# Kernel tuning notes

Hardware: AMD Instinct MI355X
Metric: run time of the kernel (lower is better)

## Reference

```python
import jax, jax.numpy as jnp
import numpy as np

B, R, C = 4, 36, 3          # batch, n_rotations, kernel_dim/output_dim
H, W = 384, 224             # padded image spatial: (320+64, 160+64)
CROP = 64
PAD = CROP // 2             # pad_size = 32


def setup_inputs() -> dict:
    key = jax.random.key(0)
    k1, k2 = jax.random.split(key)
    logits = jax.random.normal(k1, (B, C, H, W), dtype=jnp.float32)
    kernel = jax.random.normal(k2, (B * R, C, CROP, CROP), dtype=jnp.float32)
    return {"logits": logits, "kernel": kernel}


def _correlate(logits, kernel):
    # Original computes a full B x (B*R) cross-correlation via F.conv2d and then
    # discards all off-diagonal blocks. A grouped conv (feature_group_count=B)
    # computes exactly the kept diagonal blocks: group i correlates sample i's
    # feature map with that sample's R rotated kernels. interpolate/crop are
    # per-channel/per-pixel so they commute with the channel selection -> same math.
    b, c, h, w = logits.shape
    r = kernel.shape[0] // b
    x = logits.reshape(1, b * c, h, w)
    out = jax.lax.conv_general_dilated(
        x, kernel,
        window_strides=(1, 1),
        padding=[(PAD, PAD), (PAD, PAD)],
        dimension_numbers=("NCHW", "OIHW", "NCHW"),
        feature_group_count=b,
    )  # [1, b*r, h+1, w+1]  (h + 2*PAD - CROP + 1 = h + 1)
    out = out.reshape(b, r, out.shape[-2], out.shape[-1])
    # F.interpolate(..., mode='bilinear', align_corners=False) == half-pixel
    # bilinear resize without antialiasing.
    out = jax.image.resize(out, (b, r, h, w), method="bilinear", antialias=False)
    out = out[:, :, PAD:-PAD, PAD:-PAD]  # [b, r, h-2*PAD, w-2*PAD] = [b, r, 320, 160]
    hc, wc = out.shape[-2], out.shape[-1]
    # softmax over the flattened per-sample (rotation x spatial) map
    flat = jax.nn.softmax(out.reshape(b, -1), axis=-1)
    return flat.reshape(b, r, hc, wc)


def reference(logits, kernel):
    return _correlate(logits, kernel)
```

## Files before the change

### kernel.cpp

```cpp
#include <hip/hip_runtime.h>

typedef short bf16x8 __attribute__((ext_vector_type(8)));
typedef float f32x4  __attribute__((ext_vector_type(4)));
typedef unsigned short u16;

#define B_ 4
#define R_ 36
#define RP 48
#define C_ 3
#define H_ 384
#define W_ 224
#define KS 64
#define OY 321
#define OX 161
#define HC 320
#define WC 160
#define LCOLS 128
#define PITCH 88
#define CHUNK 6144
#define BLKS_PER_BATCH 7200

__device__ __forceinline__ u16 bf16rtn(float v) {
    union { float f; unsigned u; } U; U.f = v;
    unsigned r = U.u + 0x7fffu + ((U.u >> 16) & 1u);
    return (u16)(r >> 16);
}
__device__ __forceinline__ float bf16tof(u16 h) {
    union { float f; unsigned u; } U; U.u = ((unsigned)h) << 16; return U.f;
}

__device__ __forceinline__ float wave_max(float v) {
    #pragma unroll
    for (int off = 32; off > 0; off >>= 1) v = fmaxf(v, __shfl_down(v, off, 64));
    return v;
}
__device__ __forceinline__ float wave_sum(float v) {
    #pragma unroll
    for (int off = 32; off > 0; off >>= 1) v += __shfl_down(v, off, 64);
    return v;
}

__device__ __forceinline__ void dma16(const u16* g, u16* l) {
    __builtin_amdgcn_global_load_lds(
        (const __attribute__((address_space(1))) void*)g,
        (__attribute__((address_space(3))) void*)l, 16, 0, 0);
}

__global__ __launch_bounds__(256) void prep_weights(
    const float* __restrict__ wk, u16* __restrict__ wa)
{
    int d = blockIdx.x * 256 + threadIdx.x;
    int ky    = d & 63;
    int t1    = d >> 6;
    int r     = t1 % 48;
    int t2    = t1 / 48;
    int plane = t2 & 1;
    int t3    = t2 >> 1;
    int kx    = t3 & 63;
    int bc    = t3 >> 6;
    int c     = bc % 3;
    int b     = bc / 3;
    float v = 0.f;
    if (r < R_) v = wk[(((size_t)(b*R_ + r)*C_ + c)*KS + ky)*KS + kx];
    u16 h = bf16rtn(v);
    u16 o = plane ? bf16rtn(v - bf16tof(h)) : h;
    int kySw = ky ^ ((r & 7) << 3);
    wa[(size_t)t3*CHUNK + plane*3072 + r*64 + kySw] = o;
}

template<int NT>
__device__ __forceinline__ void conv_body(
    const float* __restrict__ in, const u16* __restrict__ wa,
    float* __restrict__ out, u16* Lh, u16* Ll, u16* Ab, int x0, int y0)
{
    const int b    = blockIdx.z;
    const int t    = threadIdx.x;
    const int w    = __builtin_amdgcn_readfirstlane(t >> 6);
    const int lane = t & 63;
    const int nu   = lane & 15;
    const int q    = lane >> 4;

    f32x4 acc[3][NT];
    #pragma unroll
    for (int mi = 0; mi < 3; mi++)
        #pragma unroll
        for (int n = 0; n < NT; n++)
            acc[mi][n] = (f32x4){0.f, 0.f, 0.f, 0.f};

    const u16* wbase = wa + (size_t)(b*192)*CHUNK;

    {
        const u16* src = wbase + (3*w)*512 + lane*8;
        u16* dst = Ab + (3*w)*512;
        dma16(src,        dst);
        dma16(src + 512,  dst + 512);
        dma16(src + 1024, dst + 1024);
    }

    for (int c = 0; c < C_; c++) {
        __syncthreads();
        const float* src = in + ((size_t)(b*C_ + c))*H_*W_;
        #pragma unroll
        for (int k = 0; k < 6; k++) {
            int idx = t + 256*k;
            if (idx < 1408) {
                int pair = idx >> 5;
                int r0   = pair * 2;
                int c4   = (idx & 31) * 4;
                int gx   = x0 + c4;
                int gy   = y0 + r0;
                float4 va = make_float4(0.f,0.f,0.f,0.f), vb = va;
                if (gx < W_) {
                    if (gy < H_)     va = *(const float4*)(src + (size_t)gy*W_ + gx);
                    if (gy + 1 < H_) vb = *(const float4*)(src + (size_t)(gy+1)*W_ + gx);
                }
                const float* pa = &va.x;
                const float* pb = &vb.x;
                #pragma unroll
                for (int j = 0; j < 4; j++) {
                    int col = c4 + j;
                    u16 ha = bf16rtn(pa[j]);
                    u16 hb = bf16rtn(pb[j]);
                    u16 la = bf16rtn(pa[j] - bf16tof(ha));
                    u16 lb = bf16rtn(pb[j] - bf16tof(hb));
                    *(unsigned*)&Lh[col*PITCH + r0] = (unsigned)ha | ((unsigned)hb << 16);
                    *(unsigned*)&Ll[col*PITCH + r0] = (unsigned)la | ((unsigned)lb << 16);
                }
            }
        }
        __syncthreads();

        #pragma unroll 1
        for (int kx = 0; kx < KS; kx++) {
            const int g = c*64 + kx;
            const int p = g & 1;
            __builtin_amdgcn_s_waitcnt(0x3F70);
            __builtin_amdgcn_s_barrier();
            if (g + 1 < 192) {
                const u16* s2 = wbase + (size_t)(g+1)*CHUNK + (3*w)*512 + lane*8;
                u16* d2 = Ab + (p^1)*CHUNK + (3*w)*512;
                dma16(s2,        d2);
                dma16(s2 + 512,  d2 + 512);
                dma16(s2 + 1024, d2 + 1024);
            }
            const u16* Abp = Ab + p*CHUNK;
            #pragma unroll
            for (int kycI = 0; kycI < 2; kycI++) {
                const int kyc = kycI * 32;
                bf16x8 Ah[3], Al[3];
                #pragma unroll
                for (int mi = 0; mi < 3; mi++) {
                    int off = (mi*16 + nu)*64 + ((kyc + 8*q) ^ ((nu & 7) << 3));
                    Ah[mi] = *(const bf16x8*)(Abp + off);
                    Al[mi] = *(const bf16x8*)(Abp + 3072 + off);
                }
                const u16* colbase = Lh + (size_t)(nu + kx)*PITCH + kyc + 8*q + 8*w;
                #pragma unroll
                for (int n = 0; n < NT; n++) {
                    const u16* ph = colbase + n*16*PITCH;
                    bf16x8 Bh = *(const bf16x8*)ph;
                    bf16x8 Bl = *(const bf16x8*)(ph + (size_t)LCOLS*PITCH);
                    #pragma unroll
                    for (int mi = 0; mi < 3; mi++) {
                        acc[mi][n] = __builtin_amdgcn_mfma_f32_16x16x32_bf16(Ah[mi], Bh, acc[mi][n], 0, 0, 0);
                        acc[mi][n] = __builtin_amdgcn_mfma_f32_16x16x32_bf16(Ah[mi], Bl, acc[mi][n], 0, 0, 0);
                        acc[mi][n] = __builtin_amdgcn_mfma_f32_16x16x32_bf16(Al[mi], Bh, acc[mi][n], 0, 0, 0);
                    }
                }
            }
        }
    }

    const int y = y0 + 8*w;
    if (y <= 320) {
        #pragma unroll
        for (int mi = 0; mi < 3; mi++) {
            #pragma unroll
            for (int n = 0; n < NT; n++) {
                #pragma unroll
                for (int i = 0; i < 4; i++) {
                    int r = mi*16 + q*4 + i;
                    int x = x0 + n*16 + nu;
                    if (r < R_ && x < OX)
                        out[((size_t)(b*R_ + r)*OY + y)*OX + x] = acc[mi][n][i];
                }
            }
        }
    }
}

__global__ __launch_bounds__(256) void conv_mfma(
    const float* __restrict__ in, const u16* __restrict__ wa, float* __restrict__ out)
{
    __shared__ __align__(16) u16 smem[2*LCOLS*PITCH + 2*CHUNK];
    u16* Lh = smem;
    u16* Ll = smem + LCOLS*PITCH;
    u16* Ab = smem + 2*LCOLS*PITCH;
    const int s  = blockIdx.y;
    const int y0 = (s < 80) ? (((s >> 3) << 5) + (s & 7)) : 320;

    if (blockIdx.x == 0)      conv_body<4>(in, wa, out, Lh, Ll, Ab, 0,   y0);
    else if (blockIdx.x == 1) conv_body<4>(in, wa, out, Lh, Ll, Ab, 64,  y0);
    else                      conv_body<3>(in, wa, out, Lh, Ll, Ab, 128, y0);
}

__global__ __launch_bounds__(256) void resize_kernel(
    const float* __restrict__ cv, float* __restrict__ out, float* __restrict__ pmax)
{
    const int t = threadIdx.x;
    const int idx = blockIdx.x * 256 + t;
    const int j = idx % WC;
    const int rest = idx / WC;
    const int i = rest % HC;
    const int br = rest / HC;

    float fy = (i + 32.5f) * (1.0f/384.0f);
    float fx = (j + 32.5f) * (1.0f/224.0f);

    const float* p = cv + ((size_t)br*OY + i)*OX + j;
    float v00 = p[0], v01 = p[1], v10 = p[OX], v11 = p[OX+1];
    float v = (1.f-fy)*((1.f-fx)*v00 + fx*v01) + fy*((1.f-fx)*v10 + fx*v11);
    out[idx] = v;

    __shared__ float sm[4];
    float m = wave_max(v);
    if ((t & 63) == 0) sm[t >> 6] = m;
    __syncthreads();
    if (t == 0) pmax[blockIdx.x] = fmaxf(fmaxf(sm[0], sm[1]), fmaxf(sm[2], sm[3]));
}

__global__ __launch_bounds__(256) void reduce_kernel(
    const float* __restrict__ part, float* __restrict__ res, int n, int is_sum)
{
    const int b = blockIdx.x;
    const int t = threadIdx.x;
    const float* p = part + (size_t)b*n;
    float v = is_sum ? 0.f : -3.0e38f;
    for (int k = t; k < n; k += 256) v = is_sum ? (v + p[k]) : fmaxf(v, p[k]);
    __shared__ float sm[4];
    float w = is_sum ? wave_sum(v) : wave_max(v);
    if ((t & 63) == 0) sm[t >> 6] = w;
    __syncthreads();
    if (t == 0) {
        res[b] = is_sum ? (sm[0]+sm[1]+sm[2]+sm[3])
                        : fmaxf(fmaxf(sm[0], sm[1]), fmaxf(sm[2], sm[3]));
    }
}

__global__ __launch_bounds__(256) void exp_kernel(
    float* __restrict__ out, const float* __restrict__ bmax, float* __restrict__ psum)
{
    const int t = threadIdx.x;
    const int idx = blockIdx.x * 256 + t;
    const int b = blockIdx.x / BLKS_PER_BATCH;
    float e = expf(out[idx] - bmax[b]);
    out[idx] = e;
    __shared__ float sm[4];
    float s = wave_sum(e);
    if ((t & 63) == 0) sm[t >> 6] = s;
    __syncthreads();
    if (t == 0) psum[blockIdx.x] = sm[0]+sm[1]+sm[2]+sm[3];
}

__global__ __launch_bounds__(256) void scale_kernel(
    float* __restrict__ out, const float* __restrict__ bsum)
{
    const int idx = blockIdx.x * 256 + threadIdx.x;
    const int b = blockIdx.x / BLKS_PER_BATCH;
    out[idx] = out[idx] / bsum[b];
}

extern "C" void kernel_launch(void* const* d_in, const int* in_sizes, int n_in,
                              void* d_out, int out_size, void* d_ws, size_t ws_size,
                              hipStream_t stream)
{
    const float* logits = (const float*)d_in[0];
    const float* wk     = (const float*)d_in[1];
    float* out = (float*)d_out;
    char*  wsB = (char*)d_ws;

    float* convOut = (float*)wsB;
    u16*   wa      = (u16*)(wsB + 29768256);
    float* pmax    = (float*)(wsB + 29768256 + 9437184);
    float* psum    = pmax + 28800;
    float* bmax    = psum + 28800;
    float* bsum    = bmax + 8;

    hipLaunchKernelGGL(prep_weights, dim3(18432), dim3(256), 0, stream, wk, wa);
    hipLaunchKernelGGL(conv_mfma,    dim3(3, 81, B_), dim3(256), 0, stream, logits, wa, convOut);
    hipLaunchKernelGGL(resize_kernel, dim3(28800), dim3(256), 0, stream, convOut, out, pmax);
    hipLaunchKernelGGL(reduce_kernel, dim3(4),     dim3(256), 0, stream, pmax, bmax, BLKS_PER_BATCH, 0);
    hipLaunchKernelGGL(exp_kernel,    dim3(28800), dim3(256), 0, stream, out, bmax, psum);
    hipLaunchKernelGGL(reduce_kernel, dim3(4),     dim3(256), 0, stream, psum, bsum, BLKS_PER_BATCH, 1);
    hipLaunchKernelGGL(scale_kernel,  dim3(28800), dim3(256), 0, stream, out, bsum);
}
```

Before: 703.1 us.

## Compute two output row groups per conv block to reuse weight tiles

```diff
diff --git a/kernel.cpp b/kernel.cpp
--- a/kernel.cpp
+++ b/kernel.cpp
@@ -16,8 +16,8 @@
 #define HC 320
 #define WC 160
 #define LCOLS 128
-#define PITCH 88
-#define CHUNK 6144
+#define PITCH 120
+#define GR 3072
 #define BLKS_PER_BATCH 7200
 
 __device__ __forceinline__ u16 bf16rtn(float v) {
@@ -50,22 +50,23 @@
     const float* __restrict__ wk, u16* __restrict__ wa)
 {
     int d = blockIdx.x * 256 + threadIdx.x;
-    int ky    = d & 63;
-    int t1    = d >> 6;
+    int ky32  = d & 31;
+    int t1    = d >> 5;
     int r     = t1 % 48;
     int t2    = t1 / 48;
     int plane = t2 & 1;
-    int t3    = t2 >> 1;
-    int kx    = t3 & 63;
-    int bc    = t3 >> 6;
+    int g2    = t2 >> 1;
+    int kycp  = g2 & 1;
+    int kx    = (g2 >> 1) & 63;
+    int bc    = g2 >> 7;
     int c     = bc % 3;
     int b     = bc / 3;
+    int ky    = kycp*32 + ky32;
     float v = 0.f;
     if (r < R_) v = wk[(((size_t)(b*R_ + r)*C_ + c)*KS + ky)*KS + kx];
     u16 h = bf16rtn(v);
     u16 o = plane ? bf16rtn(v - bf16tof(h)) : h;
-    int kySw = ky ^ ((r & 7) << 3);
-    wa[(size_t)t3*CHUNK + plane*3072 + r*64 + kySw] = o;
+    wa[(size_t)g2*GR + plane*1536 + r*32 + (ky32 ^ ((r & 3) << 3))] = o;
 }
 
 template<int NT>
@@ -80,30 +81,31 @@
     const int nu   = lane & 15;
     const int q    = lane >> 4;
 
-    f32x4 acc[3][NT];
+    f32x4 acc[2][3][NT];
     #pragma unroll
-    for (int mi = 0; mi < 3; mi++)
+    for (int yi = 0; yi < 2; yi++)
         #pragma unroll
-        for (int n = 0; n < NT; n++)
-            acc[mi][n] = (f32x4){0.f, 0.f, 0.f, 0.f};
-
-    const u16* wbase = wa + (size_t)(b*192)*CHUNK;
+        for (int mi = 0; mi < 3; mi++)
+            #pragma unroll
+            for (int n = 0; n < NT; n++)
+                acc[yi][mi][n] = (f32x4){0.f, 0.f, 0.f, 0.f};
+
+    const u16* gbase = wa + (size_t)(b*384)*GR;
 
     {
-        const u16* src = wbase + (3*w)*512 + lane*8;
-        u16* dst = Ab + (3*w)*512;
-        dma16(src,        dst);
-        dma16(src + 512,  dst + 512);
-        dma16(src + 1024, dst + 1024);
+        const u16* s0 = gbase + lane*8;
+        if (w < 2) { dma16(s0 + (2*w)*512, Ab + (2*w)*512);
+                     dma16(s0 + (2*w+1)*512, Ab + (2*w+1)*512); }
+        else       { dma16(s0 + (w+2)*512, Ab + (w+2)*512); }
     }
 
     for (int c = 0; c < C_; c++) {
         __syncthreads();
         const float* src = in + ((size_t)(b*C_ + c))*H_*W_;
         #pragma unroll
-        for (int k = 0; k < 6; k++) {
+        for (int k = 0; k < 8; k++) {
             int idx = t + 256*k;
-            if (idx < 1408) {
+            if (idx < 1920) {
                 int pair = idx >> 5;
                 int r0   = pair * 2;
                 int c4   = (idx & 31) * 4;
@@ -131,58 +133,62 @@
         __syncthreads();
 
         #pragma unroll 1
-        for (int kx = 0; kx < KS; kx++) {
-            const int g = c*64 + kx;
-            const int p = g & 1;
+        for (int gi = 0; gi < 128; gi++) {
+            const int g = c*128 + gi;
             __builtin_amdgcn_s_waitcnt(0x3F70);
             __builtin_amdgcn_s_barrier();
-            if (g + 1 < 192) {
-                const u16* s2 = wbase + (size_t)(g+1)*CHUNK + (3*w)*512 + lane*8;
-                u16* d2 = Ab + (p^1)*CHUNK + (3*w)*512;
-                dma16(s2,        d2);
-                dma16(s2 + 512,  d2 + 512);
-                dma16(s2 + 1024, d2 + 1024);
-            }
-            const u16* Abp = Ab + p*CHUNK;
+            if (g + 1 < 384) {
+                const u16* s2 = gbase + (size_t)(g+1)*GR + lane*8;
+                u16* d2 = Ab + ((g+1) & 1)*GR;
+                if (w < 2) { dma16(s2 + (2*w)*512, d2 + (2*w)*512);
+                             dma16(s2 + (2*w+1)*512, d2 + (2*w+1)*512); }
+                else       { dma16(s2 + (w+2)*512, d2 + (w+2)*512); }
+            }
+            const u16* Abp = Ab + (g & 1)*GR;
+            const int kx   = gi >> 1;
+            const int kycp = gi & 1;
+
+            bf16x8 Ah[3], Al[3];
             #pragma unroll
-            for (int kycI = 0; kycI < 2; kycI++) {
-                const int kyc = kycI * 32;
-                bf16x8 Ah[3], Al[3];
+            for (int mi = 0; mi < 3; mi++) {
+                int off = (mi*16 + nu)*32 + ((8*q) ^ ((nu & 3) << 3));
+                Ah[mi] = *(const bf16x8*)(Abp + off);
+                Al[mi] = *(const bf16x8*)(Abp + 1536 + off);
+            }
+            const u16* colbase = Lh + (size_t)(nu + kx)*PITCH + 32*kycp + 8*q + 8*w;
+            #pragma unroll
+            for (int n = 0; n < NT; n++) {
                 #pragma unroll
-                for (int mi = 0; mi < 3; mi++) {
-                    int off = (mi*16 + nu)*64 + ((kyc + 8*q) ^ ((nu & 7) << 3));
-                    Ah[mi] = *(const bf16x8*)(Abp + off);
-                    Al[mi] = *(const bf16x8*)(Abp + 3072 + off);
-                }
-                const u16* colbase = Lh + (size_t)(nu + kx)*PITCH + kyc + 8*q + 8*w;
-                #pragma unroll
-                for (int n = 0; n < NT; n++) {
-                    const u16* ph = colbase + n*16*PITCH;
+                for (int yi = 0; yi < 2; yi++) {
+                    const u16* ph = colbase + n*16*PITCH + 32*yi;
                     bf16x8 Bh = *(const bf16x8*)ph;
                     bf16x8 Bl = *(const bf16x8*)(ph + (size_t)LCOLS*PITCH);
                     #pragma unroll
                     for (int mi = 0; mi < 3; mi++) {
-                        acc[mi][n] = __builtin_amdgcn_mfma_f32_16x16x32_bf16(Ah[mi], Bh, acc[mi][n], 0, 0, 0);
-                        acc[mi][n] = __builtin_amdgcn_mfma_f32_16x16x32_bf16(Ah[mi], Bl, acc[mi][n], 0, 0, 0);
-                        acc[mi][n] = __builtin_amdgcn_mfma_f32_16x16x32_bf16(Al[mi], Bh, acc[mi][n], 0, 0, 0);
+                        acc[yi][mi][n] = __builtin_amdgcn_mfma_f32_16x16x32_bf16(Ah[mi], Bh, acc[yi][mi][n], 0, 0, 0);
+                        acc[yi][mi][n] = __builtin_amdgcn_mfma_f32_16x16x32_bf16(Ah[mi], Bl, acc[yi][mi][n], 0, 0, 0);
+                        acc[yi][mi][n] = __builtin_amdgcn_mfma_f32_16x16x32_bf16(Al[mi], Bh, acc[yi][mi][n], 0, 0, 0);
                     }
                 }
             }
         }
     }
 
-    const int y = y0 + 8*w;
-    if (y <= 320) {
-        #pragma unroll
-        for (int mi = 0; mi < 3; mi++) {
+    #pragma unroll
+    for (int yi = 0; yi < 2; yi++) {
+        const int y = y0 + 8*w + 32*yi;
+        if (y <= 320) {
             #pragma unroll
-            for (int n = 0; n < NT; n++) {
+            for (int mi = 0; mi < 3; mi++) {
                 #pragma unroll
-                for (int i = 0; i < 4; i++) {
-                    int r = mi*16 + q*4 + i;
-                    int x = x0 + n*16 + nu;
-                    if (r < R_ && x < OX)
-                        out[((size_t)(b*R_ + r)*OY + y)*OX + x] = acc[mi][n][i];
+                for (int n = 0; n < NT; n++) {
+                    #pragma unroll
+                    for (int i = 0; i < 4; i++) {
+                        int r = mi*16 + q*4 + i;
+                        int x = x0 + n*16 + nu;
+                        if (r < R_ && x < OX)
+                            out[((size_t)(b*R_ + r)*OY + y)*OX + x] = acc[yi][mi][n][i];
+                    }
                 }
             }
         }
@@ -192,12 +198,12 @@
 __global__ __launch_bounds__(256) void conv_mfma(
     const float* __restrict__ in, const u16* __restrict__ wa, float* __restrict__ out)
 {
-    __shared__ __align__(16) u16 smem[2*LCOLS*PITCH + 2*CHUNK];
+    __shared__ __align__(16) u16 smem[2*LCOLS*PITCH + 2*GR];
     u16* Lh = smem;
     u16* Ll = smem + LCOLS*PITCH;
     u16* Ab = smem + 2*LCOLS*PITCH;
     const int s  = blockIdx.y;
-    const int y0 = (s < 80) ? (((s >> 3) << 5) + (s & 7)) : 320;
+    const int y0 = (s < 40) ? ((s >> 3)*64 + (s & 7)) : 320;
 
     if (blockIdx.x == 0)      conv_body<4>(in, wa, out, Lh, Ll, Ab, 0,   y0);
     else if (blockIdx.x == 1) conv_body<4>(in, wa, out, Lh, Ll, Ab, 64,  y0);
@@ -287,7 +293,7 @@
     float* bsum    = bmax + 8;
 
     hipLaunchKernelGGL(prep_weights, dim3(18432), dim3(256), 0, stream, wk, wa);
-    hipLaunchKernelGGL(conv_mfma,    dim3(3, 81, B_), dim3(256), 0, stream, logits, wa, convOut);
+    hipLaunchKernelGGL(conv_mfma,    dim3(3, 41, B_), dim3(256), 0, stream, logits, wa, convOut);
     hipLaunchKernelGGL(resize_kernel, dim3(28800), dim3(256), 0, stream, convOut, out, pmax);
     hipLaunchKernelGGL(reduce_kernel, dim3(4),     dim3(256), 0, stream, pmax, bmax, BLKS_PER_BATCH, 0);
     hipLaunchKernelGGL(exp_kernel,    dim3(28800), dim3(256), 0, stream, out, bmax, psum);
```

After: 677.8 us. 1.04x faster.
